# Kernel optimization log

Hardware: AMD Instinct MI355X
Metric: run time of the kernel (lower is better)

The kernel has to match this reference:

```python
import jax, jax.numpy as jnp
import numpy as np

B_SI = 4.1491   # neutron scattering length Si (fm)
B_O = 5.803     # neutron scattering length O (fm)
CUTOFF = 3.5    # tetrahedral neighbour cutoff (A)
BIG = 1e6       # masked-distance sentinel (finite to keep grads NaN-free)


def setup_inputs() -> dict:
    key = jax.random.key(0)
    k1, k2 = jax.random.split(key)
    N, L = 4096, 40.0
    positions = jax.random.uniform(k1, (N, 3), dtype=jnp.float32) * L
    cell = (L * jnp.eye(3)).astype(jnp.float32)
    r_bins = (0.05 + 0.05 * jnp.arange(200, dtype=jnp.float32))      # 0.05..10.0 A
    q_bins = jnp.linspace(0.5, 25.0, 500, dtype=jnp.float32)          # A^-1
    species = jax.random.randint(k2, (N,), 0, 3, dtype=jnp.int32)     # 0=Si, 1/2=O
    return {"positions": positions, "cell": cell, "r_bins": r_bins,
            "q_bins": q_bins, "species": species}


def _pair_geometry(positions, cell):
    # Minimum-image displacements under a general periodic cell.
    disp = positions[:, None, :] - positions[None, :, :]        # [N,N,3]
    frac = disp @ jnp.linalg.inv(cell)
    frac = frac - jnp.round(frac)
    disp = frac @ cell
    d2 = jnp.sum(disp * disp, axis=-1)                           # [N,N]
    self_mask = jnp.eye(positions.shape[0], dtype=bool)
    dist = jnp.sqrt(jnp.where(self_mask, 1.0, d2))               # safe sqrt on diag
    return disp, dist, self_mask


def reference(positions, cell, r_bins, q_bins, species):
    N = positions.shape[0]
    nbins = r_bins.shape[0]
    dtype = positions.dtype

    disp, dist, self_mask = _pair_geometry(positions, cell)

    # --- neutron-weighted G(r): differentiable linear (cloud-in-cell) binning ---
    b = jnp.where(species == 0, B_SI, B_O).astype(dtype)         # per-atom scattering length
    w = (b[:, None] * b[None, :]) / (jnp.mean(b) ** 2)           # Faber-Ziman pair weights
    r0, dr = r_bins[0], r_bins[1] - r_bins[0]
    x = (dist - r0) / dr
    i0 = jnp.floor(x).astype(jnp.int32)
    f = x - i0.astype(dtype)
    valid = (~self_mask) & (i0 >= 0) & (i0 < nbins - 1)
    w0 = jnp.where(valid, w * (1.0 - f), 0.0).ravel()
    w1 = jnp.where(valid, w * f, 0.0).ravel()
    i0f = jnp.clip(i0, 0, nbins - 1).ravel()
    hist = (jnp.zeros(nbins, dtype)
            .at[i0f].add(w0)
            .at[jnp.clip(i0f + 1, 0, nbins - 1)].add(w1))
    V = jnp.abs(jnp.linalg.det(cell))
    rho = N / V
    shell = 4.0 * jnp.pi * r_bins ** 2 * dr                       # ideal-gas shell volume
    G_r = hist / (N * rho * shell)                                # [nbins]

    # --- total correlation function T(r) = 4 pi rho r G(r) ---
    T_r = 4.0 * jnp.pi * rho * r_bins * G_r

    # --- structure factor S(Q) = 1 + 4 pi rho int r^2 (G(r)-1) sinc(Qr) dr ---
    qr = q_bins[:, None] * r_bins[None, :]                        # [nQ, nr]
    integrand = (r_bins ** 2) * (G_r - 1.0)
    S_Q = 1.0 + 4.0 * jnp.pi * rho * dr * jnp.sum(
        integrand[None, :] * jnp.sinc(qr / jnp.pi), axis=1)

    # --- tetrahedral order parameter q_tet over Si centres with O neighbours ---
    central = species == 0
    nbr_ok = (species != 0)[None, :] & (~self_mask)
    nd = jnp.where(nbr_ok, dist, BIG)
    negd, idx = jax.lax.top_k(-nd, 4)                             # 4 nearest O per atom
    d4 = -negd                                                    # [N,4]
    u = jnp.take_along_axis(disp, idx[:, :, None], axis=1) / d4[:, :, None]  # unit vecs
    cosang = jnp.einsum('nkd,nld->nkl', u, u)                     # [N,4,4]
    pair_mask = jnp.triu(jnp.ones((4, 4), bool), 1)               # 6 angle pairs
    q_i = 1.0 - (3.0 / 8.0) * jnp.sum(((cosang + 1.0 / 3.0) ** 2) * pair_mask, axis=(1, 2))
    vf = (central & (d4[:, 3] < CUTOFF)).astype(dtype)            # needs 4 nbrs in cutoff
    q_tet = jnp.sum(q_i * vf) / jnp.maximum(jnp.sum(vf), 1.0)

    return G_r, T_r, S_Q, q_tet
```

## Files before the change

kernel.cpp:

```cpp
#include <hip/hip_runtime.h>
#include <climits>
#include <math.h>


#define B_SI_F 4.1491f
#define B_O_F  5.803f
#define CUTOFF_F 3.5f
#define NCOPIES 16

#define WS_HIST 16
#define WS_QV   4096

__device__ __forceinline__ bool dless(float da, int ia, float db, int ib) {
    return (da < db) || (da == db && ia < ib);
}

struct CellK {
    float ci0, ci1, ci2, ci3, ci4, ci5, ci6, ci7, ci8;
    float c0, c1, c2, c3, c4, c5, c6, c7, c8;
};

__device__ __forceinline__ CellK make_cell(const float* __restrict__ cellm,
                                           bool& diag) {
    CellK K;
    K.c0 = cellm[0]; K.c1 = cellm[1]; K.c2 = cellm[2];
    K.c3 = cellm[3]; K.c4 = cellm[4]; K.c5 = cellm[5];
    K.c6 = cellm[6]; K.c7 = cellm[7]; K.c8 = cellm[8];
    double m0 = K.c0, m1 = K.c1, m2 = K.c2;
    double m3 = K.c3, m4 = K.c4, m5 = K.c5;
    double m6 = K.c6, m7 = K.c7, m8 = K.c8;
    double det = m0*(m4*m8 - m5*m7) - m1*(m3*m8 - m5*m6) + m2*(m3*m7 - m4*m6);
    double rd = 1.0 / det;
    K.ci0 = (float)( (m4*m8 - m5*m7) * rd);
    K.ci1 = (float)(-(m1*m8 - m2*m7) * rd);
    K.ci2 = (float)( (m1*m5 - m2*m4) * rd);
    K.ci3 = (float)(-(m3*m8 - m5*m6) * rd);
    K.ci4 = (float)( (m0*m8 - m2*m6) * rd);
    K.ci5 = (float)(-(m0*m5 - m2*m3) * rd);
    K.ci6 = (float)( (m3*m7 - m4*m6) * rd);
    K.ci7 = (float)(-(m0*m7 - m1*m6) * rd);
    K.ci8 = (float)( (m0*m4 - m1*m3) * rd);
    diag = (K.c1 == 0.0f) && (K.c2 == 0.0f) && (K.c3 == 0.0f) &&
           (K.c5 == 0.0f) && (K.c6 == 0.0f) && (K.c7 == 0.0f);
    return K;
}

template<bool DIAG>
__device__ __forceinline__ void min_image(const CellK& K,
                                          float dx, float dy, float dz,
                                          float& ex, float& ey, float& ez) {
    if (DIAG) {
        float t0 = dx * K.ci0, t1 = dy * K.ci4, t2 = dz * K.ci8;
        t0 -= rintf(t0);  t1 -= rintf(t1);  t2 -= rintf(t2);
        ex = t0 * K.c0;  ey = t1 * K.c4;  ez = t2 * K.c8;
    } else {
        float f0 = dx*K.ci0 + dy*K.ci3 + dz*K.ci6;
        float f1 = dx*K.ci1 + dy*K.ci4 + dz*K.ci7;
        float f2 = dx*K.ci2 + dy*K.ci5 + dz*K.ci8;
        f0 -= rintf(f0);  f1 -= rintf(f1);  f2 -= rintf(f2);
        ex = f0*K.c0 + f1*K.c3 + f2*K.c6;
        ey = f0*K.c1 + f1*K.c4 + f2*K.c7;
        ez = f0*K.c2 + f1*K.c5 + f2*K.c8;
    }
}

template<bool DIAG>
__device__ __forceinline__ void hist_sweep(const CellK& K,
                                           const float4* __restrict__ sj,
                                           int lbase,
                                           float xi, float yi, float zi, float wi,
                                           float rb0, float inv_dr, int nbins_m1,
                                           float* shist) {
    #pragma unroll 4
    for (int l = 0; l < 32; ++l) {
        const float4 pj = sj[lbase + l];
        float ex, ey, ez;
        min_image<DIAG>(K, xi - pj.x, yi - pj.y, zi - pj.z, ex, ey, ez);
        float dist = __builtin_amdgcn_sqrtf(fmaf(ex, ex, fmaf(ey, ey, ez * ez)));
        float x  = (dist - rb0) * inv_dr;
        float fl = floorf(x);
        int   i0 = (int)fl;
        if (i0 >= 0 && i0 < nbins_m1) {
            float w = wi * pj.w;
            float f = x - fl;
            atomicAdd(&shist[i0],     w * (1.0f - f));
            atomicAdd(&shist[i0 + 1], w * f);
        }
    }
}

template<bool DIAG>
__device__ __forceinline__ void top4_sweep_s(const CellK& K,
                                             const float* __restrict__ pos,
                                             const int* __restrict__ species,
                                             int N, int lane,
                                             float xi, float yi, float zi,
                                             float& e0, float& e1, float& e2, float& e3,
                                             int& j0, int& j1, int& j2, int& j3) {
    #pragma unroll 4
    for (int k = lane; k < N; k += 64) {
        int   sp = species[k];
        float px = pos[3*k], py = pos[3*k+1], pz = pos[3*k+2];
        float ex, ey, ez;
        min_image<DIAG>(K, xi - px, yi - py, zi - pz, ex, ey, ez);
        float d2 = fmaf(ex, ex, fmaf(ey, ey, ez * ez));
        float c  = (sp != 0) ? d2 : 1e30f;
        int   jc = k;
        if (dless(c, jc, e3, j3)) {
            bool lt2 = dless(c, jc, e2, j2);
            bool lt1 = dless(c, jc, e1, j1);
            bool lt0 = dless(c, jc, e0, j0);
            e3 = lt2 ? e2 : c;               j3 = lt2 ? j2 : jc;
            e2 = lt2 ? (lt1 ? e1 : c) : e2;  j2 = lt2 ? (lt1 ? j1 : jc) : j2;
            e1 = lt1 ? (lt0 ? e0 : c) : e1;  j1 = lt1 ? (lt0 ? j0 : jc) : j1;
            e0 = lt0 ? c : e0;               j0 = lt0 ? jc : j0;
        }
    }
}

__global__ __launch_bounds__(256) void k_main(const float* __restrict__ cellm,
                                              const float* __restrict__ pos,
                                              const int* __restrict__ species,
                                              const float* __restrict__ rbins,
                                              float* __restrict__ ws,
                                              int N, int nbins, int T, int P2) {
    const int tid = threadIdx.x;
    const int bid = blockIdx.x;

    bool diag;
    const CellK K = make_cell(cellm, diag);

    if (bid < P2) {
        __shared__ float shist[256];
        __shared__ float sjf[64 * 4];
        shist[tid] = 0.0f;

        const int jhalf = bid & 1;
        int rem = bid >> 1;
        int ti = 0;
        while (rem >= T - ti) { rem -= T - ti; ti++; }
        const int tj = ti + rem;
        const int jb0 = tj * 128 + jhalf * 64;

        if (tid < 192) {
            int g = 3 * jb0 + tid;
            float v = (g < 3 * N) ? pos[g] : 0.0f;
            sjf[(tid / 3) * 4 + (tid % 3)] = v;
        } else {
            int a = tid - 192;
            int ja = jb0 + a;
            float b = (ja < N) ? ((species[ja] == 0) ? B_SI_F : B_O_F) : 0.0f;
            sjf[a * 4 + 3] = b;
        }

        const float rb0     = rbins[0];
        const float inv_dr  = 1.0f / (rbins[1] - rbins[0]);
        const int   nbins_m1 = nbins - 1;

        const int il  = tid & 127;
        const int sub = tid >> 7;
        const int i   = ti * 128 + il;
        const int ig  = min(i, N - 1);
        const float xi = pos[3*ig], yi = pos[3*ig+1], zi = pos[3*ig+2];
        const float b_i = (species[ig] == 0) ? B_SI_F : B_O_F;
        const float wmul = (ti == tj) ? 1.0f : 2.0f;
        const float wi = (i < N) ? b_i * wmul : 0.0f;

        __syncthreads();

        const float4* sj = (const float4*)sjf;
        if (diag) hist_sweep<true >(K, sj, sub * 32, xi, yi, zi, wi, rb0, inv_dr, nbins_m1, shist);
        else      hist_sweep<false>(K, sj, sub * 32, xi, yi, zi, wi, rb0, inv_dr, nbins_m1, shist);

        __syncthreads();

        float* gh = ws + WS_HIST + (size_t)(bid % NCOPIES) * nbins;
        for (int t = tid; t < nbins; t += 256) {
            float h = shist[t];
            if (h != 0.0f) atomicAdd(&gh[t], h);
        }
        return;
    }

    const int s = __builtin_amdgcn_readfirstlane((bid - P2) * 4 + (tid >> 6));
    if (s >= N) return;
    const int lane = tid & 63;
    float* __restrict__ qv = ws + WS_QV;

    if (species[s] != 0) {
        if (lane == 0) { qv[2*s] = 0.0f; qv[2*s + 1] = 0.0f; }
        return;
    }

    const float xi = pos[3*s], yi = pos[3*s+1], zi = pos[3*s+2];

    float e0 = 1e30f, e1 = 1e30f, e2 = 1e30f, e3 = 1e30f;
    int   j0 = INT_MAX, j1 = INT_MAX, j2 = INT_MAX, j3 = INT_MAX;

    if (diag) top4_sweep_s<true >(K, pos, species, N, lane, xi, yi, zi, e0, e1, e2, e3, j0, j1, j2, j3);
    else      top4_sweep_s<false>(K, pos, species, N, lane, xi, yi, zi, e0, e1, e2, e3, j0, j1, j2, j3);

    float r0d, r1d, r2d, r3d;  int r0j, r1j, r2j, r3j;
    #define EXTRACT_MIN(RD, RJ)                                        \
    {                                                                  \
        float md = e0; int mj = j0;                                    \
        for (int off = 32; off > 0; off >>= 1) {                       \
            float od = __shfl_xor(md, off, 64);                        \
            int   oj = __shfl_xor(mj, off, 64);                        \
            bool keep = dless(md, mj, od, oj);                         \
            md = keep ? md : od;                                       \
            mj = keep ? mj : oj;                                       \
        }                                                              \
        RD = md; RJ = mj;                                              \
        bool pop = (j0 == mj);                                         \
        e0 = pop ? e1 : e0;  j0 = pop ? j1 : j0;                       \
        e1 = pop ? e2 : e1;  j1 = pop ? j2 : j1;                       \
        e2 = pop ? e3 : e2;  j2 = pop ? j3 : j2;                       \
        e3 = pop ? 1e30f : e3;  j3 = pop ? INT_MAX : j3;               \
    }
    EXTRACT_MIN(r0d, r0j)
    EXTRACT_MIN(r1d, r1j)
    EXTRACT_MIN(r2d, r2j)
    EXTRACT_MIN(r3d, r3j)
    #undef EXTRACT_MIN

    if (lane == 0) {
        float qiv = 0.0f, vf = 0.0f;
        float dd0 = sqrtf(r0d), dd1 = sqrtf(r1d), dd2 = sqrtf(r2d), dd3 = sqrtf(r3d);
        if (dd3 < CUTOFF_F) {
            float ux[4], uy[4], uz[4];
            float dd[4]  = {dd0, dd1, dd2, dd3};
            int   jj4[4] = {r0j, r1j, r2j, r3j};
            #pragma unroll
            for (int k = 0; k < 4; ++k) {
                int jk = jj4[k];
                float ex, ey, ez;
                if (diag) min_image<true >(K, xi - pos[3*jk], yi - pos[3*jk+1], zi - pos[3*jk+2], ex, ey, ez);
                else      min_image<false>(K, xi - pos[3*jk], yi - pos[3*jk+1], zi - pos[3*jk+2], ex, ey, ez);
                ux[k] = ex / dd[k];
                uy[k] = ey / dd[k];
                uz[k] = ez / dd[k];
            }
            float s2 = 0.0f;
            #pragma unroll
            for (int k = 0; k < 4; ++k)
                #pragma unroll
                for (int l = k + 1; l < 4; ++l) {
                    float cs = ux[k]*ux[l] + uy[k]*uy[l] + uz[k]*uz[l];
                    float t  = cs + (1.0f / 3.0f);
                    s2 += t * t;
                }
            qiv = 1.0f - 0.375f * s2;
            vf  = 1.0f;
        }
        qv[2*s]     = qiv;
        qv[2*s + 1] = vf;
    }
}

__device__ __forceinline__ float fast_sinc(float x) {
    float rev = x * 0.15915494309189535f;
    rev -= rintf(rev);
    float sn = __builtin_amdgcn_sinf(rev);
    return sn * __builtin_amdgcn_rcpf(x);
}

__global__ __launch_bounds__(256) void k_finalize(const float* __restrict__ cellm,
                                                  const float* __restrict__ ws,
                                                  const float* __restrict__ rbins,
                                                  const float* __restrict__ qbins,
                                                  const int* __restrict__ species,
                                                  float* __restrict__ out,
                                                  int N, int nbins, int nq) {
    __shared__ float2 srw[256];
    __shared__ float rq[256], rv[256];
    __shared__ int   scnt[256];
    const int tid = threadIdx.x;

    double m0 = cellm[0], m1 = cellm[1], m2 = cellm[2];
    double m3 = cellm[3], m4 = cellm[4], m5 = cellm[5];
    double m6 = cellm[6], m7 = cellm[7], m8 = cellm[8];
    double det = m0*(m4*m8 - m5*m7) - m1*(m3*m8 - m5*m6) + m2*(m3*m7 - m4*m6);
    const float rho = (float)((double)N / fabs(det));

    {
        int c = 0;
        for (int k = tid; k < N; k += 256) c += (species[k] == 0) ? 1 : 0;
        scnt[tid] = c;
    }
    __syncthreads();
    for (int s = 128; s > 0; s >>= 1) {
        if (tid < s) scnt[tid] += scnt[tid + s];
        __syncthreads();
    }
    const int nSi = scnt[0];
    const float mean_b  = ((float)nSi * B_SI_F + (float)(N - nSi) * B_O_F) / (float)N;
    const float w_scale = 1.0f / (mean_b * mean_b);

    const float dr  = rbins[1] - rbins[0];
    const float FOURPI = 4.0f * 3.14159265358979323846f;

    for (int t = tid; t < nbins; t += blockDim.x) {
        float h = 0.0f;
        #pragma unroll
        for (int c = 0; c < NCOPIES; ++c) h += ws[WS_HIST + c * nbins + t];
        h *= w_scale;
        float r = rbins[t];
        float shell = FOURPI * r * r * dr;
        float g = h / ((float)N * rho * shell);
        srw[t] = make_float2(r, r * r * (g - 1.0f));
        if (blockIdx.x == 0) {
            out[t] = g;
            out[nbins + t] = FOURPI * rho * r * g;
        }
    }

    if (blockIdx.x == 0) {
        const float* qv = ws + WS_QV;
        float sq = 0.0f, sv = 0.0f;
        for (int s = tid; s < N; s += 256) {
            sq += qv[2*s];
            sv += qv[2*s + 1];
        }
        rq[tid] = sq; rv[tid] = sv;
    }
    __syncthreads();
    if (blockIdx.x == 0) {
        for (int s = 128; s > 0; s >>= 1) {
            if (tid < s) { rq[tid] += rq[tid + s]; rv[tid] += rv[tid + s]; }
            __syncthreads();
        }
        if (tid == 0)
            out[2 * nbins + nq] = rq[0] / fmaxf(rv[0], 1.0f);
    }

    int q = blockIdx.x * blockDim.x + tid;
    if (q < nq) {
        float qq = qbins[q];
        float s0 = 0.0f, s1 = 0.0f, s2 = 0.0f, s3 = 0.0f;
        int t = 0;
        for (; t + 4 <= nbins; t += 4) {
            float2 a = srw[t], b = srw[t+1], c = srw[t+2], d = srw[t+3];
            s0 += a.y * fast_sinc(qq * a.x);
            s1 += b.y * fast_sinc(qq * b.x);
            s2 += c.y * fast_sinc(qq * c.x);
            s3 += d.y * fast_sinc(qq * d.x);
        }
        for (; t < nbins; ++t) {
            float2 a = srw[t];
            s0 += a.y * fast_sinc(qq * a.x);
        }
        float s = (s0 + s1) + (s2 + s3);
        out[2 * nbins + q] = 1.0f + FOURPI * rho * dr * s;
    }
}

extern "C" void kernel_launch(void* const* d_in, const int* in_sizes, int n_in,
                              void* d_out, int out_size, void* d_ws, size_t ws_size,
                              hipStream_t stream) {
    const float* pos     = (const float*)d_in[0];
    const float* cell    = (const float*)d_in[1];
    const float* rbins   = (const float*)d_in[2];
    const float* qbins   = (const float*)d_in[3];
    const int*   species = (const int*)d_in[4];
    float* out = (float*)d_out;
    float* ws  = (float*)d_ws;

    const int N     = in_sizes[4];
    const int nbins = in_sizes[2];
    const int nq    = in_sizes[3];

    const int T  = (N + 127) / 128;
    const int P2 = T * (T + 1);
    const int BT = (N + 3) / 4;

    k_main<<<P2 + BT, 256, 0, stream>>>(cell, pos, species, rbins, ws, N, nbins, T, P2);
    k_finalize<<<(nq + 255) / 256, 256, 0, stream>>>(cell, ws, rbins, qbins, species, out, N, nbins, nq);
}
```

Before: 108.8 us.

## Fuse finalize into main kernel via last-block-done atomic counter

Merges the histogram/top-4 kernel and the finalize kernel into one launch. Each block increments a global counter when it finishes, and the last block to arrive computes G(r), T(r), S(Q) and q_tet. This removes a kernel launch and the gap between kernels, but it adds a memset launch to reset the counter. The S(Q) loop over 500 q values now runs in a single block instead of two, so that tail work is serialized.

```diff
diff --git a/kernel.cpp b/kernel.cpp
--- a/kernel.cpp
+++ b/kernel.cpp
@@ -8,6 +8,7 @@
 #define CUTOFF_F 3.5f
 #define NCOPIES 16
 
+#define WS_CNT  0
 #define WS_HIST 16
 #define WS_QV   4096
 
@@ -118,21 +119,36 @@
     }
 }
 
-__global__ __launch_bounds__(256) void k_main(const float* __restrict__ cellm,
-                                              const float* __restrict__ pos,
-                                              const int* __restrict__ species,
-                                              const float* __restrict__ rbins,
-                                              float* __restrict__ ws,
-                                              int N, int nbins, int T, int P2) {
+__device__ __forceinline__ float fast_sinc(float x) {
+    float rev = x * 0.15915494309189535f;
+    rev -= rintf(rev);
+    float sn = __builtin_amdgcn_sinf(rev);
+    return sn * __builtin_amdgcn_rcpf(x);
+}
+
+__global__ __launch_bounds__(256) void k_all(const float* __restrict__ cellm,
+                                             const float* __restrict__ pos,
+                                             const int* __restrict__ species,
+                                             const float* __restrict__ rbins,
+                                             const float* __restrict__ qbins,
+                                             float* __restrict__ ws,
+                                             float* __restrict__ out,
+                                             int N, int nbins, int nq,
+                                             int T, int P2, int TOTAL) {
     const int tid = threadIdx.x;
     const int bid = blockIdx.x;
 
+    __shared__ float  shist[256];
+    __shared__ float  sjf[256];
+    __shared__ float2 srw[256];
+    __shared__ float  rq[256], rv[256];
+    __shared__ int    scnt[256];
+    __shared__ int    slast;
+
     bool diag;
     const CellK K = make_cell(cellm, diag);
 
     if (bid < P2) {
-        __shared__ float shist[256];
-        __shared__ float sjf[64 * 4];
         shist[tid] = 0.0f;
 
         const int jhalf = bid & 1;
@@ -179,109 +195,92 @@
             float h = shist[t];
             if (h != 0.0f) atomicAdd(&gh[t], h);
         }
-        return;
-    }
-
-    const int s = __builtin_amdgcn_readfirstlane((bid - P2) * 4 + (tid >> 6));
-    if (s >= N) return;
-    const int lane = tid & 63;
-    float* __restrict__ qv = ws + WS_QV;
-
-    if (species[s] != 0) {
-        if (lane == 0) { qv[2*s] = 0.0f; qv[2*s + 1] = 0.0f; }
-        return;
-    }
-
-    const float xi = pos[3*s], yi = pos[3*s+1], zi = pos[3*s+2];
-
-    float e0 = 1e30f, e1 = 1e30f, e2 = 1e30f, e3 = 1e30f;
-    int   j0 = INT_MAX, j1 = INT_MAX, j2 = INT_MAX, j3 = INT_MAX;
-
-    if (diag) top4_sweep_s<true >(K, pos, species, N, lane, xi, yi, zi, e0, e1, e2, e3, j0, j1, j2, j3);
-    else      top4_sweep_s<false>(K, pos, species, N, lane, xi, yi, zi, e0, e1, e2, e3, j0, j1, j2, j3);
-
-    float r0d, r1d, r2d, r3d;  int r0j, r1j, r2j, r3j;
-    #define EXTRACT_MIN(RD, RJ)                                        \
-    {                                                                  \
-        float md = e0; int mj = j0;                                    \
-        for (int off = 32; off > 0; off >>= 1) {                       \
-            float od = __shfl_xor(md, off, 64);                        \
-            int   oj = __shfl_xor(mj, off, 64);                        \
-            bool keep = dless(md, mj, od, oj);                         \
-            md = keep ? md : od;                                       \
-            mj = keep ? mj : oj;                                       \
-        }                                                              \
-        RD = md; RJ = mj;                                              \
-        bool pop = (j0 == mj);                                         \
-        e0 = pop ? e1 : e0;  j0 = pop ? j1 : j0;                       \
-        e1 = pop ? e2 : e1;  j1 = pop ? j2 : j1;                       \
-        e2 = pop ? e3 : e2;  j2 = pop ? j3 : j2;                       \
-        e3 = pop ? 1e30f : e3;  j3 = pop ? INT_MAX : j3;               \
-    }
-    EXTRACT_MIN(r0d, r0j)
-    EXTRACT_MIN(r1d, r1j)
-    EXTRACT_MIN(r2d, r2j)
-    EXTRACT_MIN(r3d, r3j)
-    #undef EXTRACT_MIN
-
-    if (lane == 0) {
-        float qiv = 0.0f, vf = 0.0f;
-        float dd0 = sqrtf(r0d), dd1 = sqrtf(r1d), dd2 = sqrtf(r2d), dd3 = sqrtf(r3d);
-        if (dd3 < CUTOFF_F) {
-            float ux[4], uy[4], uz[4];
-            float dd[4]  = {dd0, dd1, dd2, dd3};
-            int   jj4[4] = {r0j, r1j, r2j, r3j};
-            #pragma unroll
-            for (int k = 0; k < 4; ++k) {
-                int jk = jj4[k];
-                float ex, ey, ez;
-                if (diag) min_image<true >(K, xi - pos[3*jk], yi - pos[3*jk+1], zi - pos[3*jk+2], ex, ey, ez);
-                else      min_image<false>(K, xi - pos[3*jk], yi - pos[3*jk+1], zi - pos[3*jk+2], ex, ey, ez);
-                ux[k] = ex / dd[k];
-                uy[k] = ey / dd[k];
-                uz[k] = ez / dd[k];
+    } else {
+        const int s = __builtin_amdgcn_readfirstlane((bid - P2) * 4 + (tid >> 6));
+        const int lane = tid & 63;
+        float* __restrict__ qv = ws + WS_QV;
+
+        if (s < N) {
+            if (species[s] != 0) {
+                if (lane == 0) { qv[2*s] = 0.0f; qv[2*s + 1] = 0.0f; }
+            } else {
+                const float xi = pos[3*s], yi = pos[3*s+1], zi = pos[3*s+2];
+
+                float e0 = 1e30f, e1 = 1e30f, e2 = 1e30f, e3 = 1e30f;
+                int   j0 = INT_MAX, j1 = INT_MAX, j2 = INT_MAX, j3 = INT_MAX;
+
+                if (diag) top4_sweep_s<true >(K, pos, species, N, lane, xi, yi, zi, e0, e1, e2, e3, j0, j1, j2, j3);
+                else      top4_sweep_s<false>(K, pos, species, N, lane, xi, yi, zi, e0, e1, e2, e3, j0, j1, j2, j3);
+
+                float r0d, r1d, r2d, r3d;  int r0j, r1j, r2j, r3j;
+                #define EXTRACT_MIN(RD, RJ)                                        \
+                {                                                                  \
+                    float md = e0; int mj = j0;                                    \
+                    for (int off = 32; off > 0; off >>= 1) {                       \
+                        float od = __shfl_xor(md, off, 64);                        \
+                        int   oj = __shfl_xor(mj, off, 64);                        \
+                        bool keep = dless(md, mj, od, oj);                         \
+                        md = keep ? md : od;                                       \
+                        mj = keep ? mj : oj;                                       \
+                    }                                                              \
+                    RD = md; RJ = mj;                                              \
+                    bool pop = (j0 == mj);                                         \
+                    e0 = pop ? e1 : e0;  j0 = pop ? j1 : j0;                       \
+                    e1 = pop ? e2 : e1;  j1 = pop ? j2 : j1;                       \
+                    e2 = pop ? e3 : e2;  j2 = pop ? j3 : j2;                       \
+                    e3 = pop ? 1e30f : e3;  j3 = pop ? INT_MAX : j3;               \
+                }
+                EXTRACT_MIN(r0d, r0j)
+                EXTRACT_MIN(r1d, r1j)
+                EXTRACT_MIN(r2d, r2j)
+                EXTRACT_MIN(r3d, r3j)
+                #undef EXTRACT_MIN
+
+                if (lane == 0) {
+                    float qiv = 0.0f, vf = 0.0f;
+                    float dd0 = sqrtf(r0d), dd1 = sqrtf(r1d), dd2 = sqrtf(r2d), dd3 = sqrtf(r3d);
+                    if (dd3 < CUTOFF_F) {
+                        float ux[4], uy[4], uz[4];
+                        float dd[4]  = {dd0, dd1, dd2, dd3};
+                        int   jj4[4] = {r0j, r1j, r2j, r3j};
+                        #pragma unroll
+                        for (int k = 0; k < 4; ++k) {
+                            int jk = jj4[k];
+                            float ex, ey, ez;
+                            if (diag) min_image<true >(K, xi - pos[3*jk], yi - pos[3*jk+1], zi - pos[3*jk+2], ex, ey, ez);
+                            else      min_image<false>(K, xi - pos[3*jk], yi - pos[3*jk+1], zi - pos[3*jk+2], ex, ey, ez);
+                            ux[k] = ex / dd[k];
+                            uy[k] = ey / dd[k];
+                            uz[k] = ez / dd[k];
+                        }
+                        float s2 = 0.0f;
+                        #pragma unroll
+                        for (int k = 0; k < 4; ++k)
+                            #pragma unroll
+                            for (int l = k + 1; l < 4; ++l) {
+                                float cs = ux[k]*ux[l] + uy[k]*uy[l] + uz[k]*uz[l];
+                                float t  = cs + (1.0f / 3.0f);
+                                s2 += t * t;
+                            }
+                        qiv = 1.0f - 0.375f * s2;
+                        vf  = 1.0f;
+                    }
+                    qv[2*s]     = qiv;
+                    qv[2*s + 1] = vf;
+                }
             }
-            float s2 = 0.0f;
-            #pragma unroll
-            for (int k = 0; k < 4; ++k)
-                #pragma unroll
-                for (int l = k + 1; l < 4; ++l) {
-                    float cs = ux[k]*ux[l] + uy[k]*uy[l] + uz[k]*uz[l];
-                    float t  = cs + (1.0f / 3.0f);
-                    s2 += t * t;
-                }
-            qiv = 1.0f - 0.375f * s2;
-            vf  = 1.0f;
-        }
-        qv[2*s]     = qiv;
-        qv[2*s + 1] = vf;
-    }
-}
-
-__device__ __forceinline__ float fast_sinc(float x) {
-    float rev = x * 0.15915494309189535f;
-    rev -= rintf(rev);
-    float sn = __builtin_amdgcn_sinf(rev);
-    return sn * __builtin_amdgcn_rcpf(x);
-}
-
-__global__ __launch_bounds__(256) void k_finalize(const float* __restrict__ cellm,
-                                                  const float* __restrict__ ws,
-                                                  const float* __restrict__ rbins,
-                                                  const float* __restrict__ qbins,
-                                                  const int* __restrict__ species,
-                                                  float* __restrict__ out,
-                                                  int N, int nbins, int nq) {
-    __shared__ float2 srw[256];
-    __shared__ float rq[256], rv[256];
-    __shared__ int   scnt[256];
-    const int tid = threadIdx.x;
-
-    double m0 = cellm[0], m1 = cellm[1], m2 = cellm[2];
-    double m3 = cellm[3], m4 = cellm[4], m5 = cellm[5];
-    double m6 = cellm[6], m7 = cellm[7], m8 = cellm[8];
-    double det = m0*(m4*m8 - m5*m7) - m1*(m3*m8 - m5*m6) + m2*(m3*m7 - m4*m6);
-    const float rho = (float)((double)N / fabs(det));
+        }
+    }
+
+    __syncthreads();
+    if (tid == 0) {
+        __threadfence();
+        unsigned old = atomicAdd((unsigned*)&((int*)ws)[WS_CNT], 1u);
+        slast = (old == (unsigned)(TOTAL - 1)) ? 1 : 0;
+    }
+    __syncthreads();
+    if (!slast) return;
+    __threadfence();
 
     {
         int c = 0;
@@ -297,10 +296,16 @@
     const float mean_b  = ((float)nSi * B_SI_F + (float)(N - nSi) * B_O_F) / (float)N;
     const float w_scale = 1.0f / (mean_b * mean_b);
 
+    double m0 = K.c0, m1 = K.c1, m2 = K.c2;
+    double m3 = K.c3, m4 = K.c4, m5 = K.c5;
+    double m6 = K.c6, m7 = K.c7, m8 = K.c8;
+    double det = m0*(m4*m8 - m5*m7) - m1*(m3*m8 - m5*m6) + m2*(m3*m7 - m4*m6);
+    const float rho = (float)((double)N / fabs(det));
+
     const float dr  = rbins[1] - rbins[0];
     const float FOURPI = 4.0f * 3.14159265358979323846f;
 
-    for (int t = tid; t < nbins; t += blockDim.x) {
+    for (int t = tid; t < nbins; t += 256) {
         float h = 0.0f;
         #pragma unroll
         for (int c = 0; c < NCOPIES; ++c) h += ws[WS_HIST + c * nbins + t];
@@ -309,13 +314,11 @@
         float shell = FOURPI * r * r * dr;
         float g = h / ((float)N * rho * shell);
         srw[t] = make_float2(r, r * r * (g - 1.0f));
-        if (blockIdx.x == 0) {
-            out[t] = g;
-            out[nbins + t] = FOURPI * rho * r * g;
-        }
-    }
-
-    if (blockIdx.x == 0) {
+        out[t] = g;
+        out[nbins + t] = FOURPI * rho * r * g;
+    }
+
+    {
         const float* qv = ws + WS_QV;
         float sq = 0.0f, sv = 0.0f;
         for (int s = tid; s < N; s += 256) {
@@ -325,17 +328,14 @@
         rq[tid] = sq; rv[tid] = sv;
     }
     __syncthreads();
-    if (blockIdx.x == 0) {
-        for (int s = 128; s > 0; s >>= 1) {
-            if (tid < s) { rq[tid] += rq[tid + s]; rv[tid] += rv[tid + s]; }
-            __syncthreads();
-        }
-        if (tid == 0)
-            out[2 * nbins + nq] = rq[0] / fmaxf(rv[0], 1.0f);
-    }
-
-    int q = blockIdx.x * blockDim.x + tid;
-    if (q < nq) {
+    for (int s = 128; s > 0; s >>= 1) {
+        if (tid < s) { rq[tid] += rq[tid + s]; rv[tid] += rv[tid + s]; }
+        __syncthreads();
+    }
+    if (tid == 0)
+        out[2 * nbins + nq] = rq[0] / fmaxf(rv[0], 1.0f);
+
+    for (int q = tid; q < nq; q += 256) {
         float qq = qbins[q];
         float s0 = 0.0f, s1 = 0.0f, s2 = 0.0f, s3 = 0.0f;
         int t = 0;
@@ -373,7 +373,9 @@
     const int T  = (N + 127) / 128;
     const int P2 = T * (T + 1);
     const int BT = (N + 3) / 4;
-
-    k_main<<<P2 + BT, 256, 0, stream>>>(cell, pos, species, rbins, ws, N, nbins, T, P2);
-    k_finalize<<<(nq + 255) / 256, 256, 0, stream>>>(cell, ws, rbins, qbins, species, out, N, nbins, nq);
-}
+    const int TOTAL = P2 + BT;
+
+    hipMemsetAsync(d_ws, 0, 4, stream);
+    k_all<<<TOTAL, 256, 0, stream>>>(cell, pos, species, rbins, qbins, ws, out,
+                                     N, nbins, nq, T, P2, TOTAL);
+}
```

Measured after the change: 140.2 us. 1.29x slower.
